# Kernel tuning notes

Measured on AMD Instinct MI355X. Metric: run time of the kernel, lower is better.

The kernel has to match this reference:

```python
import jax, jax.numpy as jnp
import numpy as np

B, S, H, D = 4, 2048, 8, 64


def init_offset(size, a=0.02, b=0.1, lo=8.0, hi=14.0):
    if size == 1:
        return jnp.array([(hi - lo) / 2], dtype=jnp.float32)
    x = jnp.log(jnp.expm1(jnp.linspace(a, b, size)))
    x = (x - x.min()) / (x.max() - x.min())
    return (x * abs(hi - lo) + lo).astype(jnp.float32)


def setup_inputs() -> dict:
    key = jax.random.key(0)
    k1, k2, k3 = jax.random.split(key, 3)
    qk = jax.random.normal(k1, (B, S, 2, H, D), dtype=jnp.float32)
    v = jax.random.normal(k2, (B, S, H, D), dtype=jnp.float32)
    n = jax.random.normal(k3, (B, S, H), dtype=jnp.float32)
    offset = init_offset(H)  # learned per-head offset parameter
    return {"qk": qk, "v": v, "n": n, "offset": offset}


def reference(qk, v, n, offset):
    # approx_fn = elu(x) + 1 (feature map), norm_fn = softplus, scale_B=True
    q = jax.nn.elu(qk[:, :, 0]) + 1.0  # (B,S,H,D)
    k = jax.nn.elu(qk[:, :, 1]) + 1.0  # (B,S,H,D)
    scale = 1.0 / jnp.sqrt(jnp.asarray(q.shape[-1], q.dtype))
    # outer product per position then causal prefix-sum over sequence
    kv = jnp.einsum('bshd,bsht->bshdt', k * scale, v)  # (B,S,H,D,D)
    kv = jnp.cumsum(kv, axis=1)
    out = jnp.einsum('bshd,bshdt->bsht', q, kv)  # (B,S,H,D)
    norm = jnp.exp(-jax.nn.softplus(n + offset))  # (B,S,H)
    return norm[:, :, :, None] * out
```

## Files before the change

kernel.cpp:

```cpp
#include <hip/hip_runtime.h>
#include <cstdint>

#define BB 4
#define SS 2048
#define HH 8
#define DD 64
#define CC 64
#define NCK (SS/CC)
#define BHH (BB*HH)

typedef __attribute__((ext_vector_type(8))) short  short8;
typedef __attribute__((ext_vector_type(4))) float  f32x4;
typedef __attribute__((ext_vector_type(4))) unsigned short us4;

__device__ __forceinline__ float elu1(float x) {
    return x > 0.f ? x + 1.f : __expf(x);
}
__device__ __forceinline__ unsigned short f2bf(float f) {
    unsigned int u = __float_as_uint(f);
    u += 0x7FFFu + ((u >> 16) & 1u);
    return (unsigned short)(u >> 16);
}
__device__ __forceinline__ float bf2f(unsigned short h) {
    return __uint_as_float(((unsigned int)h) << 16);
}
#define SWZ(r,c) ((r) * DD + ((c) ^ (((r) & 7) << 3)))

template<int M0, int M1>
__device__ __forceinline__ void xpose4(float v[4], int lane) {
    {
        const bool hi = (lane & M0) != 0;
        float x0 = hi ? v[0] : v[1];
        float x1 = hi ? v[2] : v[3];
        float r0 = __shfl_xor(x0, M0);
        float r1 = __shfl_xor(x1, M0);
        if (hi) { v[0] = r0; v[2] = r1; } else { v[1] = r0; v[3] = r1; }
    }
    {
        const bool hi = (lane & M1) != 0;
        float x0 = hi ? v[0] : v[2];
        float x1 = hi ? v[1] : v[3];
        float r0 = __shfl_xor(x0, M1);
        float r1 = __shfl_xor(x1, M1);
        if (hi) { v[0] = r0; v[1] = r1; } else { v[2] = r0; v[3] = r1; }
    }
}

__device__ __forceinline__ unsigned long long pack4bf(const float v[4]) {
    unsigned long long r;
    r  = (unsigned long long)f2bf(v[0]);
    r |= (unsigned long long)f2bf(v[1]) << 16;
    r |= (unsigned long long)f2bf(v[2]) << 32;
    r |= (unsigned long long)f2bf(v[3]) << 48;
    return r;
}

__global__ __launch_bounds__(256) void kv_chunk_kernel(
    const float* __restrict__ qk, const float* __restrict__ v,
    unsigned short* __restrict__ Sws, unsigned short* __restrict__ vtws)
{
    const int blk = blockIdx.x;
    const int bh = blk / NCK, c = blk % NCK;
    const int b = bh / HH, h = bh % HH;
    const int s0 = c * CC;

    __shared__ unsigned short kT[CC * DD];
    __shared__ unsigned short vT[CC * DD];

    const int tid = threadIdx.x, lane = tid & 63;

#pragma unroll
    for (int iter = 0; iter < 4; ++iter) {
        const int it = iter * 256 + tid;
        const int r = it >> 4, c0 = (it & 15) * 4;
        const int g = lane >> 4;
        const int rb = r - g;

        float4 fk = *reinterpret_cast<const float4*>(
            qk + (((size_t)(b * SS + s0 + r) * 2 + 1) * HH + h) * DD + c0);
        float kv4[4] = { elu1(fk.x) * 0.125f, elu1(fk.y) * 0.125f,
                         elu1(fk.z) * 0.125f, elu1(fk.w) * 0.125f };
        xpose4<16, 32>(kv4, lane);
        *reinterpret_cast<unsigned long long*>(&kT[SWZ(c0 + g, rb)]) = pack4bf(kv4);

        float4 fv = *reinterpret_cast<const float4*>(
            v + ((size_t)(b * SS + s0 + r) * HH + h) * DD + c0);
        float vv4[4] = { fv.x, fv.y, fv.z, fv.w };
        xpose4<16, 32>(vv4, lane);
        *reinterpret_cast<unsigned long long*>(&vT[SWZ(c0 + g, rb)]) = pack4bf(vv4);
    }
    __syncthreads();

#pragma unroll
    for (int j = 0; j < 2; ++j) {
        const int slot = j * 256 + tid;
        const int r = slot >> 3, c0 = (slot & 7) * 8;
        short8 val = *reinterpret_cast<const short8*>(&vT[SWZ(r, c0)]);
        *reinterpret_cast<short8*>(vtws + (size_t)blk * 4096 + slot * 8) = val;
    }

    const int lr = lane & 15, lk = (lane >> 4) * 8;
    const int wid = tid >> 6, mbase = wid * 16;
    f32x4 acc[4] = {};
#pragma unroll
    for (int kk = 0; kk < 2; ++kk) {
        short8 a = *reinterpret_cast<const short8*>(&vT[SWZ(mbase + lr, kk * 32 + lk)]);
#pragma unroll
        for (int nb = 0; nb < 4; ++nb) {
            short8 bk = *reinterpret_cast<const short8*>(&kT[SWZ(nb * 16 + lr, kk * 32 + lk)]);
            acc[nb] = __builtin_amdgcn_mfma_f32_16x16x32_bf16(a, bk, acc[nb], 0, 0, 0);
        }
    }

    const int crow = (lane >> 4) * 4;
#pragma unroll
    for (int nb = 0; nb < 4; ++nb) {
        float cv[4] = { acc[nb][0], acc[nb][1], acc[nb][2], acc[nb][3] };
        xpose4<1, 2>(cv, lane);
        const int t  = mbase + crow + (lane & 3);
        const int d0 = nb * 16 + (lr & ~3);
        *reinterpret_cast<unsigned long long*>(
            Sws + (size_t)blk * 4096 + t * 64 + d0) = pack4bf(cv);
    }
}

__global__ __launch_bounds__(256) void prefix_kernel(unsigned short* __restrict__ Sws)
{
    const int bh = blockIdx.x >> 4, part = blockIdx.x & 15;
    const int e = part * 256 + threadIdx.x;
    unsigned short* p = Sws + (size_t)bh * NCK * 4096 + e;

    unsigned short vals[NCK];
#pragma unroll
    for (int c = 0; c < NCK; ++c) vals[c] = p[(size_t)c * 4096];
    float run = 0.f;
#pragma unroll
    for (int c = 0; c < NCK; ++c) {
        p[(size_t)c * 4096] = f2bf(run);
        run += bf2f(vals[c]);
    }
}

__global__ __launch_bounds__(256) void out_kernel(
    const float* __restrict__ qk, const float* __restrict__ nrm,
    const float* __restrict__ offset,
    const unsigned short* __restrict__ Sws, const unsigned short* __restrict__ vtws,
    float* __restrict__ out)
{
    const int blk = blockIdx.x;
    const int bh = blk / NCK, c = blk % NCK;
    const int b = bh / HH, h = bh % HH;
    const int s0 = c * CC;

    __shared__ unsigned short qb[CC * DD];
    __shared__ unsigned short kb[CC * DD];
    __shared__ unsigned short st[CC * DD];
    __shared__ unsigned short vt[CC * DD];

    const int tid = threadIdx.x;

#pragma unroll
    for (int iter = 0; iter < 4; ++iter) {
        const int it = iter * 256 + tid;
        const int r = it >> 4, c0 = (it & 15) * 4;
        const size_t qrow = (((size_t)(b * SS + s0 + r) * 2 + 0) * HH + h) * DD;
        const size_t krow = (((size_t)(b * SS + s0 + r) * 2 + 1) * HH + h) * DD;

        float4 fq = *reinterpret_cast<const float4*>(qk + qrow + c0);
        us4 uq; uq.x = f2bf(elu1(fq.x)); uq.y = f2bf(elu1(fq.y));
                uq.z = f2bf(elu1(fq.z)); uq.w = f2bf(elu1(fq.w));
        *reinterpret_cast<us4*>(&qb[SWZ(r, c0)]) = uq;

        float4 fk = *reinterpret_cast<const float4*>(qk + krow + c0);
        us4 uk; uk.x = f2bf(elu1(fk.x) * 0.125f); uk.y = f2bf(elu1(fk.y) * 0.125f);
                uk.z = f2bf(elu1(fk.z) * 0.125f); uk.w = f2bf(elu1(fk.w) * 0.125f);
        *reinterpret_cast<us4*>(&kb[SWZ(r, c0)]) = uk;
    }
#pragma unroll
    for (int j = 0; j < 2; ++j) {
        const int slot = j * 256 + tid;
        const int r = slot >> 3, c0 = (slot & 7) * 8;
        *reinterpret_cast<short8*>(&st[SWZ(r, c0)]) =
            *reinterpret_cast<const short8*>(Sws + (size_t)blk * 4096 + slot * 8);
        *reinterpret_cast<short8*>(&vt[SWZ(r, c0)]) =
            *reinterpret_cast<const short8*>(vtws + (size_t)blk * 4096 + slot * 8);
    }
    __syncthreads();

    const int lane  = tid & 63;
    const int wid   = tid >> 6;
    const int lr    = lane & 15;
    const int lk    = (lane >> 4) * 8;
    const int mbase = wid * 16;
    const int crow  = (lane >> 4) * 4;

    short8 aq0 = *reinterpret_cast<const short8*>(&qb[SWZ(mbase + lr, lk)]);
    short8 aq1 = *reinterpret_cast<const short8*>(&qb[SWZ(mbase + lr, 32 + lk)]);

    f32x4 acc[4] = {};
    f32x4 as4[4] = {};

#pragma unroll
    for (int kk = 0; kk < 2; ++kk) {
        const short8 aq = kk ? aq1 : aq0;
#pragma unroll
        for (int nb = 0; nb < 4; ++nb) {
            short8 bs = *reinterpret_cast<const short8*>(&st[SWZ(nb * 16 + lr, kk * 32 + lk)]);
            acc[nb] = __builtin_amdgcn_mfma_f32_16x16x32_bf16(aq, bs, acc[nb], 0, 0, 0);
            short8 bk = *reinterpret_cast<const short8*>(&kb[SWZ(nb * 16 + lr, kk * 32 + lk)]);
            as4[nb] = __builtin_amdgcn_mfma_f32_16x16x32_bf16(aq, bk, as4[nb], 0, 0, 0);
        }
    }

    __syncthreads();

#pragma unroll
    for (int nb = 0; nb < 4; ++nb) {
#pragma unroll
        for (int r = 0; r < 4; ++r) {
            const int s_loc = mbase + crow + r;
            const int s2    = nb * 16 + lr;
            const float val = (s2 <= s_loc) ? as4[nb][r] : 0.f;
            st[SWZ(s_loc, s2)] = f2bf(val);
        }
    }
    __syncthreads();

    short8 aA0 = *reinterpret_cast<const short8*>(&st[SWZ(mbase + lr, lk)]);
    short8 aA1 = *reinterpret_cast<const short8*>(&st[SWZ(mbase + lr, 32 + lk)]);
#pragma unroll
    for (int kk = 0; kk < 2; ++kk) {
        const short8 aa = kk ? aA1 : aA0;
#pragma unroll
        for (int nb = 0; nb < 4; ++nb) {
            short8 bv = *reinterpret_cast<const short8*>(&vt[SWZ(nb * 16 + lr, kk * 32 + lk)]);
            acc[nb] = __builtin_amdgcn_mfma_f32_16x16x32_bf16(aa, bv, acc[nb], 0, 0, 0);
        }
    }

    const float off = offset[h];
    float nv[4];
#pragma unroll
    for (int r = 0; r < 4; ++r) {
        const int s = s0 + mbase + crow + r;
        nv[r] = 1.f / (1.f + __expf(nrm[(size_t)(b * SS + s) * HH + h] + off));
    }
#pragma unroll
    for (int nb = 0; nb < 4; ++nb) {
#pragma unroll
        for (int r = 0; r < 4; ++r) {
            const int s = s0 + mbase + crow + r;
            out[((size_t)(b * SS + s) * HH + h) * DD + nb * 16 + lr] = acc[nb][r] * nv[r];
        }
    }
}

extern "C" void kernel_launch(void* const* d_in, const int* in_sizes, int n_in,
                              void* d_out, int out_size, void* d_ws, size_t ws_size,
                              hipStream_t stream) {
    const float* qk     = (const float*)d_in[0];
    const float* v      = (const float*)d_in[1];
    const float* nrm    = (const float*)d_in[2];
    const float* offset = (const float*)d_in[3];
    float* out = (float*)d_out;

    unsigned short* Sws  = (unsigned short*)d_ws;
    unsigned short* vtws = Sws + (size_t)BHH * NCK * 4096;

    kv_chunk_kernel<<<dim3(BHH * NCK), dim3(256), 0, stream>>>(qk, v, Sws, vtws);
    prefix_kernel<<<dim3(BHH * 16), dim3(256), 0, stream>>>(Sws);
    out_kernel<<<dim3(BHH * NCK), dim3(256), 0, stream>>>(qk, nrm, offset, Sws, vtws, out);
}
```

Measured before the change: 110.3 us.

## Precompute swizzled bf16 q/k tiles and stream them into LDS via global_load_lds

The first kernel now also writes elu-transformed q and scaled k as pre-swizzled bf16 tiles to workspace, and stores vT and S in swizzled LDS order. The output kernel then copies all four tiles straight into shared memory with direct global-to-LDS loads instead of re-reading and converting fp32 qk. The prefix kernel is vectorized to handle four elements per thread, and one barrier is removed by writing the masked score matrix into the k buffer. This trades extra workspace writes in the first kernel for a lighter, conversion-free load phase in the output kernel.

```diff
diff --git a/kernel.cpp b/kernel.cpp
--- a/kernel.cpp
+++ b/kernel.cpp
@@ -57,15 +57,16 @@
 
 __global__ __launch_bounds__(256) void kv_chunk_kernel(
     const float* __restrict__ qk, const float* __restrict__ v,
-    unsigned short* __restrict__ Sws, unsigned short* __restrict__ vtws)
+    unsigned short* __restrict__ qws, unsigned short* __restrict__ kws,
+    unsigned short* __restrict__ vtws, unsigned short* __restrict__ Sws)
 {
     const int blk = blockIdx.x;
     const int bh = blk / NCK, c = blk % NCK;
     const int b = bh / HH, h = bh % HH;
     const int s0 = c * CC;
 
-    __shared__ unsigned short kT[CC * DD];
-    __shared__ unsigned short vT[CC * DD];
+    __shared__ __align__(16) unsigned short kT[CC * DD];
+    __shared__ __align__(16) unsigned short vT[CC * DD];
 
     const int tid = threadIdx.x, lane = tid & 63;
 
@@ -76,10 +77,19 @@
         const int g = lane >> 4;
         const int rb = r - g;
 
-        float4 fk = *reinterpret_cast<const float4*>(
-            qk + (((size_t)(b * SS + s0 + r) * 2 + 1) * HH + h) * DD + c0);
+        const size_t qrow = (((size_t)(b * SS + s0 + r) * 2 + 0) * HH + h) * DD;
+
+        float4 fq = *reinterpret_cast<const float4*>(qk + qrow + c0);
+        us4 uq; uq.x = f2bf(elu1(fq.x)); uq.y = f2bf(elu1(fq.y));
+                uq.z = f2bf(elu1(fq.z)); uq.w = f2bf(elu1(fq.w));
+        *reinterpret_cast<us4*>(qws + (size_t)blk * 4096 + SWZ(r, c0)) = uq;
+
+        float4 fk = *reinterpret_cast<const float4*>(qk + qrow + (size_t)HH * DD + c0);
         float kv4[4] = { elu1(fk.x) * 0.125f, elu1(fk.y) * 0.125f,
                          elu1(fk.z) * 0.125f, elu1(fk.w) * 0.125f };
+        us4 uk; uk.x = f2bf(kv4[0]); uk.y = f2bf(kv4[1]);
+                uk.z = f2bf(kv4[2]); uk.w = f2bf(kv4[3]);
+        *reinterpret_cast<us4*>(kws + (size_t)blk * 4096 + SWZ(r, c0)) = uk;
         xpose4<16, 32>(kv4, lane);
         *reinterpret_cast<unsigned long long*>(&kT[SWZ(c0 + g, rb)]) = pack4bf(kv4);
 
@@ -94,57 +104,54 @@
 #pragma unroll
     for (int j = 0; j < 2; ++j) {
         const int slot = j * 256 + tid;
-        const int r = slot >> 3, c0 = (slot & 7) * 8;
-        short8 val = *reinterpret_cast<const short8*>(&vT[SWZ(r, c0)]);
-        *reinterpret_cast<short8*>(vtws + (size_t)blk * 4096 + slot * 8) = val;
+        *reinterpret_cast<short8*>(vtws + (size_t)blk * 4096 + slot * 8) =
+            *reinterpret_cast<const short8*>(&vT[slot * 8]);
     }
 
     const int lr = lane & 15, lk = (lane >> 4) * 8;
     const int wid = tid >> 6, mbase = wid * 16;
-    f32x4 acc[4] = {};
+    f32x4 sc[4] = {};
 #pragma unroll
     for (int kk = 0; kk < 2; ++kk) {
         short8 a = *reinterpret_cast<const short8*>(&vT[SWZ(mbase + lr, kk * 32 + lk)]);
 #pragma unroll
         for (int nb = 0; nb < 4; ++nb) {
             short8 bk = *reinterpret_cast<const short8*>(&kT[SWZ(nb * 16 + lr, kk * 32 + lk)]);
-            acc[nb] = __builtin_amdgcn_mfma_f32_16x16x32_bf16(a, bk, acc[nb], 0, 0, 0);
-        }
-    }
-
+            sc[nb] = __builtin_amdgcn_mfma_f32_16x16x32_bf16(a, bk, sc[nb], 0, 0, 0);
+        }
+    }
     const int crow = (lane >> 4) * 4;
 #pragma unroll
     for (int nb = 0; nb < 4; ++nb) {
-        float cv[4] = { acc[nb][0], acc[nb][1], acc[nb][2], acc[nb][3] };
+        float cv[4] = { sc[nb][0], sc[nb][1], sc[nb][2], sc[nb][3] };
         xpose4<1, 2>(cv, lane);
         const int t  = mbase + crow + (lane & 3);
         const int d0 = nb * 16 + (lr & ~3);
         *reinterpret_cast<unsigned long long*>(
-            Sws + (size_t)blk * 4096 + t * 64 + d0) = pack4bf(cv);
+            Sws + (size_t)blk * 4096 + SWZ(t, d0)) = pack4bf(cv);
     }
 }
 
 __global__ __launch_bounds__(256) void prefix_kernel(unsigned short* __restrict__ Sws)
 {
-    const int bh = blockIdx.x >> 4, part = blockIdx.x & 15;
-    const int e = part * 256 + threadIdx.x;
+    const int bh = blockIdx.x >> 2, part = blockIdx.x & 3;
+    const int e = part * 1024 + threadIdx.x * 4;
     unsigned short* p = Sws + (size_t)bh * NCK * 4096 + e;
 
-    unsigned short vals[NCK];
-#pragma unroll
-    for (int c = 0; c < NCK; ++c) vals[c] = p[(size_t)c * 4096];
-    float run = 0.f;
+    float r0 = 0.f, r1 = 0.f, r2 = 0.f, r3 = 0.f;
 #pragma unroll
     for (int c = 0; c < NCK; ++c) {
-        p[(size_t)c * 4096] = f2bf(run);
-        run += bf2f(vals[c]);
+        us4 a = *reinterpret_cast<const us4*>(p + (size_t)c * 4096);
+        us4 o; o.x = f2bf(r0); o.y = f2bf(r1); o.z = f2bf(r2); o.w = f2bf(r3);
+        *reinterpret_cast<us4*>(p + (size_t)c * 4096) = o;
+        r0 += bf2f(a.x); r1 += bf2f(a.y); r2 += bf2f(a.z); r3 += bf2f(a.w);
     }
 }
 
 __global__ __launch_bounds__(256) void out_kernel(
-    const float* __restrict__ qk, const float* __restrict__ nrm,
-    const float* __restrict__ offset,
-    const unsigned short* __restrict__ Sws, const unsigned short* __restrict__ vtws,
+    const unsigned short* __restrict__ qws, const unsigned short* __restrict__ kws,
+    const unsigned short* __restrict__ vtws, const unsigned short* __restrict__ Sws,
+    const float* __restrict__ nrm, const float* __restrict__ offset,
     float* __restrict__ out)
 {
     const int blk = blockIdx.x;
@@ -152,57 +159,54 @@
     const int b = bh / HH, h = bh % HH;
     const int s0 = c * CC;
 
-    __shared__ unsigned short qb[CC * DD];
-    __shared__ unsigned short kb[CC * DD];
-    __shared__ unsigned short st[CC * DD];
-    __shared__ unsigned short vt[CC * DD];
-
-    const int tid = threadIdx.x;
-
-#pragma unroll
-    for (int iter = 0; iter < 4; ++iter) {
-        const int it = iter * 256 + tid;
-        const int r = it >> 4, c0 = (it & 15) * 4;
-        const size_t qrow = (((size_t)(b * SS + s0 + r) * 2 + 0) * HH + h) * DD;
-        const size_t krow = (((size_t)(b * SS + s0 + r) * 2 + 1) * HH + h) * DD;
-
-        float4 fq = *reinterpret_cast<const float4*>(qk + qrow + c0);
-        us4 uq; uq.x = f2bf(elu1(fq.x)); uq.y = f2bf(elu1(fq.y));
-                uq.z = f2bf(elu1(fq.z)); uq.w = f2bf(elu1(fq.w));
-        *reinterpret_cast<us4*>(&qb[SWZ(r, c0)]) = uq;
-
-        float4 fk = *reinterpret_cast<const float4*>(qk + krow + c0);
-        us4 uk; uk.x = f2bf(elu1(fk.x) * 0.125f); uk.y = f2bf(elu1(fk.y) * 0.125f);
-                uk.z = f2bf(elu1(fk.z) * 0.125f); uk.w = f2bf(elu1(fk.w) * 0.125f);
-        *reinterpret_cast<us4*>(&kb[SWZ(r, c0)]) = uk;
-    }
-#pragma unroll
-    for (int j = 0; j < 2; ++j) {
-        const int slot = j * 256 + tid;
-        const int r = slot >> 3, c0 = (slot & 7) * 8;
-        *reinterpret_cast<short8*>(&st[SWZ(r, c0)]) =
-            *reinterpret_cast<const short8*>(Sws + (size_t)blk * 4096 + slot * 8);
-        *reinterpret_cast<short8*>(&vt[SWZ(r, c0)]) =
-            *reinterpret_cast<const short8*>(vtws + (size_t)blk * 4096 + slot * 8);
-    }
-    __syncthreads();
-
-    const int lane  = tid & 63;
-    const int wid   = tid >> 6;
+    __shared__ __align__(16) unsigned short qb[CC * DD];
+    __shared__ __align__(16) unsigned short kb[CC * DD];
+    __shared__ __align__(16) unsigned short vT[CC * DD];
+    __shared__ __align__(16) unsigned short st[CC * DD];
+
+    const int tid = threadIdx.x, lane = tid & 63;
+    const int wid = tid >> 6;
+
+    {
+        const unsigned short* gsrc[4] = {
+            qws + (size_t)blk * 4096, kws + (size_t)blk * 4096,
+            vtws + (size_t)blk * 4096, Sws + (size_t)blk * 4096 };
+        unsigned short* ldst[4] = { qb, kb, vT, st };
+#pragma unroll
+        for (int bu = 0; bu < 4; ++bu) {
+#pragma unroll
+            for (int j = 0; j < 2; ++j) {
+                const unsigned short* gp = gsrc[bu] + (size_t)(j * 256 + tid) * 8;
+                __builtin_amdgcn_global_load_lds(
+                    (const __attribute__((address_space(1))) void*)gp,
+                    (__attribute__((address_space(3))) void*)(ldst[bu] + j * 2048 + wid * 512),
+                    16, 0, 0);
+            }
+        }
+    }
+
     const int lr    = lane & 15;
     const int lk    = (lane >> 4) * 8;
     const int mbase = wid * 16;
     const int crow  = (lane >> 4) * 4;
 
-    short8 aq0 = *reinterpret_cast<const short8*>(&qb[SWZ(mbase + lr, lk)]);
-    short8 aq1 = *reinterpret_cast<const short8*>(&qb[SWZ(mbase + lr, 32 + lk)]);
+    const float off = offset[h];
+    float nv[4];
+#pragma unroll
+    for (int r = 0; r < 4; ++r) {
+        const int s = s0 + mbase + crow + r;
+        nv[r] = nrm[(size_t)(b * SS + s) * HH + h] + off;
+    }
+#pragma unroll
+    for (int r = 0; r < 4; ++r) nv[r] = 1.f / (1.f + __expf(nv[r]));
+
+    __syncthreads();
 
     f32x4 acc[4] = {};
     f32x4 as4[4] = {};
-
 #pragma unroll
     for (int kk = 0; kk < 2; ++kk) {
-        const short8 aq = kk ? aq1 : aq0;
+        short8 aq = *reinterpret_cast<const short8*>(&qb[SWZ(mbase + lr, kk * 32 + lk)]);
 #pragma unroll
         for (int nb = 0; nb < 4; ++nb) {
             short8 bs = *reinterpret_cast<const short8*>(&st[SWZ(nb * 16 + lr, kk * 32 + lk)]);
@@ -211,7 +215,6 @@
             as4[nb] = __builtin_amdgcn_mfma_f32_16x16x32_bf16(aq, bk, as4[nb], 0, 0, 0);
         }
     }
-
     __syncthreads();
 
 #pragma unroll
@@ -221,30 +224,20 @@
             const int s_loc = mbase + crow + r;
             const int s2    = nb * 16 + lr;
             const float val = (s2 <= s_loc) ? as4[nb][r] : 0.f;
-            st[SWZ(s_loc, s2)] = f2bf(val);
-        }
-    }
-    __syncthreads();
-
-    short8 aA0 = *reinterpret_cast<const short8*>(&st[SWZ(mbase + lr, lk)]);
-    short8 aA1 = *reinterpret_cast<const short8*>(&st[SWZ(mbase + lr, 32 + lk)]);
+            kb[SWZ(s_loc, s2)] = f2bf(val);
+        }
+    }
+
 #pragma unroll
     for (int kk = 0; kk < 2; ++kk) {
-        const short8 aa = kk ? aA1 : aA0;
+        short8 aa = *reinterpret_cast<const short8*>(&kb[SWZ(mbase + lr, kk * 32 + lk)]);
 #pragma unroll
         for (int nb = 0; nb < 4; ++nb) {
-            short8 bv = *reinterpret_cast<const short8*>(&vt[SWZ(nb * 16 + lr, kk * 32 + lk)]);
+            short8 bv = *reinterpret_cast<const short8*>(&vT[SWZ(nb * 16 + lr, kk * 32 + lk)]);
             acc[nb] = __builtin_amdgcn_mfma_f32_16x16x32_bf16(aa, bv, acc[nb], 0, 0, 0);
         }
     }
 
-    const float off = offset[h];
-    float nv[4];
-#pragma unroll
-    for (int r = 0; r < 4; ++r) {
-        const int s = s0 + mbase + crow + r;
-        nv[r] = 1.f / (1.f + __expf(nrm[(size_t)(b * SS + s) * HH + h] + off));
-    }
 #pragma unroll
     for (int nb = 0; nb < 4; ++nb) {
 #pragma unroll
@@ -264,10 +257,13 @@
     const float* offset = (const float*)d_in[3];
     float* out = (float*)d_out;
 
-    unsigned short* Sws  = (unsigned short*)d_ws;
-    unsigned short* vtws = Sws + (size_t)BHH * NCK * 4096;
-
-    kv_chunk_kernel<<<dim3(BHH * NCK), dim3(256), 0, stream>>>(qk, v, Sws, vtws);
-    prefix_kernel<<<dim3(BHH * 16), dim3(256), 0, stream>>>(Sws);
-    out_kernel<<<dim3(BHH * NCK), dim3(256), 0, stream>>>(qk, nrm, offset, Sws, vtws, out);
-}
+    const size_t TILE = (size_t)BHH * NCK * 4096;
+    unsigned short* qws  = (unsigned short*)d_ws;
+    unsigned short* kws  = qws  + TILE;
+    unsigned short* vtws = kws  + TILE;
+    unsigned short* Sws  = vtws + TILE;
+
+    kv_chunk_kernel<<<dim3(BHH * NCK), dim3(256), 0, stream>>>(qk, v, qws, kws, vtws, Sws);
+    prefix_kernel<<<dim3(BHH * 4), dim3(256), 0, stream>>>(Sws);
+    out_kernel<<<dim3(BHH * NCK), dim3(256), 0, stream>>>(qws, kws, vtws, Sws, nrm, offset, out);
+}
```

New measurement: 112.7 us. +2.1%, slower.
